# Performance work log

Measured on AMD Instinct MI355X. Metric: run time of the kernel, lower is better.

## Reference

```python
import jax, jax.numpy as jnp
import numpy as np

T, B, IN, OUT = 32, 16, 64, 64
L, W, S = 4096, 64, 3          # mem_length, mem_width, shifting_size
READ_SIZE = W + 3 + S           # k, beta, g, gamma, s
WRITE_SIZE = W + 3 + S + 2 * W  # addressing params + erase + add


def setup_inputs() -> dict:
    key = jax.random.key(0)
    k1, k2 = jax.random.split(key)
    inputs = jax.random.normal(k1, (T, B, IN), dtype=jnp.float32)
    Wc = jax.random.normal(k2, (IN + OUT + W, OUT + READ_SIZE + WRITE_SIZE), dtype=jnp.float32) * 0.05
    bc = jnp.zeros((OUT + READ_SIZE + WRITE_SIZE,), dtype=jnp.float32)
    return {"inputs": inputs, "Wc": Wc, "bc": bc}


def _get_w(params, w_prev, memory):
    # params: [B, W+3+S]; w_prev: [B, L]; memory: [B, L, W]
    k = params[:, :W]
    beta = jax.nn.softplus(params[:, W])[:, None]
    g = jax.nn.sigmoid(params[:, W + 1])[:, None]
    gamma = jax.nn.softplus(params[:, W + 2])[:, None] + 1.0
    s = jax.nn.softmax(params[:, -S:], axis=-1)
    eps = 1e-14
    norm_k = jnp.sqrt(jnp.sum(k * k, axis=-1, keepdims=True) + eps)    # [B,1]
    norm_mem = jnp.sqrt(jnp.sum(memory * memory, axis=-1) + eps)       # [B,L]
    K = jnp.einsum('blw,bw->bl', memory, k) / (norm_mem * norm_k)      # cosine sim
    w_c = jax.nn.softmax(K * beta, axis=-1)
    w_g = w_c * g + (1.0 - g) * w_prev
    # circular shift: w_tilde[i] = sum_j s[j] * w_g[(i + j - left) mod L]
    left = S // 2
    shifted = jnp.stack([jnp.roll(w_g, left - j, axis=1) for j in range(S)], axis=-1)  # [B,L,S]
    w_tilde = jnp.einsum('bls,bs->bl', shifted, s)
    w = jnp.power(w_tilde, gamma)   # sharpen, gamma >= 1
    return w / jnp.sum(w, axis=1, keepdims=True)


def reference(inputs, Wc, bc):
    Bsz = inputs.shape[1]
    r0 = jnp.zeros((Bsz, W), jnp.float32)
    o0 = jnp.zeros((Bsz, OUT), jnp.float32)
    w0 = jnp.zeros((Bsz, L), jnp.float32).at[:, 0].set(1.0)  # one-hot init weights
    m0 = jnp.zeros((Bsz, L, W), jnp.float32)

    def step(carry, x_t):
        r, out, rw, ww, mem = carry
        co = jnp.concatenate([x_t, out, r], axis=1) @ Wc + bc  # linear controller
        out = co[:, :OUT]
        rp = co[:, OUT:OUT + READ_SIZE]
        wp = co[:, -WRITE_SIZE:]
        # read head (uses pre-write memory)
        rw = _get_w(rp, rw, mem)
        r = jnp.einsum('blw,bl->bw', mem, rw)
        # write head: address with same memory, then erase/add
        ww = _get_w(wp[:, :-2 * W], ww, mem)
        e = jax.nn.sigmoid(wp[:, -2 * W:-W])
        a = wp[:, -W:]
        mem = mem * (1.0 - ww[:, :, None] * e[:, None, :]) + ww[:, :, None] * a[:, None, :]
        return (r, out, rw, ww, mem), out

    _, outs = jax.lax.scan(step, (r0, o0, w0, w0, m0), inputs)
    return outs  # [T, B, OUT]
```

## Files before the change

### kernel.cpp

```cpp
#include <hip/hip_runtime.h>

#define T_STEPS 32
#define BATCH   16
#define NBPB    8
#define NBLK    (BATCH * NBPB)
#define NTHR    1024
#define LSL     512
#define MSTR    65
#define NIN     192
#define CO      332

#define OFF_CTR   0
#define OFF_SSUM  512
#define OFF_RSUM  (OFF_SSUM + BATCH * T_STEPS * 4)
#define OFF_HE    (OFF_RSUM + BATCH * T_STEPS * 64)
#define OFF_HP    (OFF_HE + BATCH * T_STEPS * NBPB * 4)
#define COMM_FLOATS (OFF_HP + BATCH * (T_STEPS + 1) * NBPB * 4)

__device__ __forceinline__ float waveSum(float v) {
#pragma unroll
  for (int off = 32; off > 0; off >>= 1) v += __shfl_xor(v, off, 64);
  return v;
}
__device__ __forceinline__ float sigmoidf(float x) { return 1.f / (1.f + __expf(-x)); }
__device__ __forceinline__ float softplusf(float x) { return x > 15.f ? x : log1pf(__expf(x)); }
__device__ __forceinline__ float aload(const float* p) {
  return __hip_atomic_load(p, __ATOMIC_RELAXED, __HIP_MEMORY_SCOPE_AGENT);
}
__device__ __forceinline__ void astore(float* p, float v) {
  __hip_atomic_store(p, v, __ATOMIC_RELAXED, __HIP_MEMORY_SCOPE_AGENT);
}

__device__ __forceinline__ void gbar(unsigned* c, unsigned expected) {
  __syncthreads();
  if (threadIdx.x == 0) {
    atomicAdd(c, 1u);
    while (__hip_atomic_load(c, __ATOMIC_RELAXED, __HIP_MEMORY_SCOPE_AGENT) < expected)
      __builtin_amdgcn_s_sleep(1);
  }
  __syncthreads();
}

__global__ void __launch_bounds__(NTHR, 1) ntm_kernel(
    const float* __restrict__ inp, const float* __restrict__ Wc,
    const float* __restrict__ bcv, float* __restrict__ dout,
    float* __restrict__ comm)
{
  const int b   = blockIdx.x & 15;
  const int g   = blockIdx.x >> 4;
  const int tid = threadIdx.x;
  const int wv  = tid >> 6;
  const int lane = tid & 63;

  __shared__ float mem[LSL * MSTR];
  __shared__ float wpR[LSL], wpW[LSL];
  __shared__ float wbR[LSL], wbW[LSL];
  __shared__ float erR[LSL], erW[LSL];
  __shared__ float xin[NIN], kr[64], kw[64], psc[12], elds[64], alds[64];
  __shared__ float outb[2][64], scrA[16], scrB[16], red[8], rpart[64];
  __shared__ float edge[8], coef[12];

  unsigned* ctr = (unsigned*)comm + b * 32;

  for (int i = tid; i < LSL * MSTR; i += NTHR) mem[i] = 0.f;
  if (tid < LSL) { wpR[tid] = 0.f; wpW[tid] = 0.f; }
  if (g == 0 && tid == 0) { wpR[0] = 1.f; wpW[0] = 1.f; }
  if (tid < 64) { outb[0][tid] = 0.f; outb[1][tid] = 0.f; }
  {
    float* hp0 = comm + OFF_HP + ((size_t)(b * (T_STEPS + 1) + 0) * NBPB + g) * 4;
    if (tid == 0)       { float v = (g == 0) ? 1.f : 0.f; astore(hp0 + 0, v); astore(hp0 + 2, v); }
    if (tid == LSL - 1) { astore(hp0 + 1, 0.f); astore(hp0 + 3, 0.f); }
  }
  unsigned expct = NBPB;
  gbar(ctr, expct);

  for (int t = 0; t < T_STEPS; ++t) {
    float* sS  = comm + OFF_SSUM + (size_t)(b * T_STEPS + t) * 4;
    float* rS  = comm + OFF_RSUM + (size_t)(b * T_STEPS + t) * 64;
    float* hE  = comm + OFF_HE + ((size_t)(b * T_STEPS + t) * NBPB + g) * 4;
    float* hPn = comm + OFF_HP + ((size_t)(b * (T_STEPS + 1) + t + 1) * NBPB + g) * 4;

    if (tid < 64)       xin[tid] = inp[((size_t)t * BATCH + b) * 64 + tid];
    else if (tid < 128) xin[tid] = outb[(t + 1) & 1][tid - 64];
    else if (tid < 192) {
      if (t == 0) xin[tid] = 0.f;
      else {
        const float* sP = comm + OFF_SSUM + (size_t)(b * T_STEPS + t - 1) * 4;
        const float* rP = comm + OFF_RSUM + (size_t)(b * T_STEPS + t - 1) * 64;
        xin[tid] = aload(rP + (tid - 128)) / aload(sP + 2);
      }
    }
    __syncthreads();

    if (tid < 2 * CO) {
      const int col = tid >> 1, h = tid & 1;
      float acc = h ? 0.f : bcv[col];
      const float* wcp = Wc + col + (size_t)(96 * h) * CO;
#pragma unroll 8
      for (int i = 0; i < 96; ++i) acc = fmaf(xin[96 * h + i], wcp[(size_t)i * CO], acc);
      acc += __shfl_xor(acc, 1, 64);
      if (h == 0) {
        if (col < 64) {
          outb[t & 1][col] = acc;
          if (g == 0) dout[((size_t)t * BATCH + b) * 64 + col] = acc;
        }
        else if (col < 128) kr[col - 64] = acc;
        else if (col < 134) psc[col - 128] = acc;
        else if (col < 198) kw[col - 134] = acc;
        else if (col < 204) psc[6 + (col - 198)] = acc;
        else if (col < 268) elds[col - 204] = sigmoidf(acc);
        else                alds[col - 268] = acc;
      }
    }
    __syncthreads();
    if (wv == 0)      { float v = kr[lane]; float s = waveSum(v * v); if (!lane) red[4] = 1.f / sqrtf(s + 1e-14f); }
    else if (wv == 1) { float v = kw[lane]; float s = waveSum(v * v); if (!lane) red[5] = 1.f / sqrtf(s + 1e-14f); }
    else if (wv == 2 && !lane) { red[6] = softplusf(psc[0]); red[7] = softplusf(psc[6]); }
    __syncthreads();

    {
      const float invnkR = red[4], invnkW = red[5];
      const float betaR = red[6], betaW = red[7];
      const int l = tid >> 1, h = tid & 1;
      const int base = l * MSTR + 32 * h;
      const float* krh = kr + 32 * h;
      const float* kwh = kw + 32 * h;
      float ss = 0.f, dr = 0.f, dw = 0.f;
#pragma unroll 8
      for (int i = 0; i < 32; ++i) {
        float v = mem[base + i];
        ss = fmaf(v, v, ss); dr = fmaf(v, krh[i], dr); dw = fmaf(v, kwh[i], dw);
      }
      ss += __shfl_xor(ss, 1, 64);
      dr += __shfl_xor(dr, 1, 64);
      dw += __shfl_xor(dw, 1, 64);
      float rinv = rsqrtf(ss + 1e-14f);
      float eRv = __expf(betaR * (dr * rinv * invnkR - 1.f));
      float eWv = __expf(betaW * (dw * rinv * invnkW - 1.f));
      if (h == 0) {
        erR[l] = eRv; erW[l] = eWv;
        if (l == 0)       { astore(hE + 0, eRv); astore(hE + 2, eWv); }
        if (l == LSL - 1) { astore(hE + 1, eRv); astore(hE + 3, eWv); }
      }
      float sRl = h ? 0.f : eRv, sWl = h ? 0.f : eWv;
      sRl = waveSum(sRl); sWl = waveSum(sWl);
      if (!lane) { scrA[wv] = sRl; scrB[wv] = sWl; }
      __syncthreads();
      if (tid == 0) {
        float a = 0.f, bb = 0.f;
        for (int j = 0; j < 16; ++j) { a += scrA[j]; bb += scrB[j]; }
        atomicAdd(sS + 0, a); atomicAdd(sS + 1, bb);
      }
    }
    expct += NBPB; gbar(ctr, expct);

    {
      const int gm = (g + NBPB - 1) & 7, gp = (g + 1) & 7;
      if (tid == 0) {
        float invSR = 1.f / aload(sS + 0), invSW = 1.f / aload(sS + 1);
        float gR = sigmoidf(psc[1]); coef[0] = gR * invSR; coef[1] = 1.f - gR;
        coef[2] = softplusf(psc[2]) + 1.f;
        float x0 = psc[3], x1 = psc[4], x2 = psc[5];
        float mx = fmaxf(x0, fmaxf(x1, x2));
        float e0 = __expf(x0 - mx), e1 = __expf(x1 - mx), e2 = __expf(x2 - mx);
        float es = 1.f / (e0 + e1 + e2);
        coef[3] = e0 * es; coef[4] = e1 * es; coef[5] = e2 * es;
        float gW = sigmoidf(psc[7]); coef[6] = gW * invSW; coef[7] = 1.f - gW;
        coef[8] = softplusf(psc[8]) + 1.f;
        float y0 = psc[9], y1 = psc[10], y2 = psc[11];
        float my = fmaxf(y0, fmaxf(y1, y2));
        float f0 = __expf(y0 - my), f1 = __expf(y1 - my), f2 = __expf(y2 - my);
        float fs = 1.f / (f0 + f1 + f2);
        coef[9] = f0 * fs; coef[10] = f1 * fs; coef[11] = f2 * fs;
      }
      if (tid == 1) {
        const float* hEm = comm + OFF_HE + ((size_t)(b * T_STEPS + t) * NBPB + gm) * 4;
        const float* hPm = comm + OFF_HP + ((size_t)(b * (T_STEPS + 1) + t) * NBPB + gm) * 4;
        edge[0] = aload(hEm + 1); edge[1] = aload(hEm + 3);
        edge[2] = aload(hPm + 1); edge[3] = aload(hPm + 3);
      }
      if (tid == 2) {
        const float* hEp = comm + OFF_HE + ((size_t)(b * T_STEPS + t) * NBPB + gp) * 4;
        const float* hPp = comm + OFF_HP + ((size_t)(b * (T_STEPS + 1) + t) * NBPB + gp) * 4;
        edge[4] = aload(hEp + 0); edge[5] = aload(hEp + 2);
        edge[6] = aload(hPp + 0); edge[7] = aload(hPp + 2);
      }
      __syncthreads();

      float pRl = 0.f, pWl = 0.f;
      if (tid < LSL) {
        const float aR = coef[0], bR = coef[1], gaR = coef[2];
        const float sr0 = coef[3], sr1 = coef[4], sr2 = coef[5];
        const float aW = coef[6], bW = coef[7], gaW = coef[8];
        const float sw0 = coef[9], sw1 = coef[10], sw2 = coef[11];

        float erm = tid ? erR[tid - 1] : edge[0];
        float ewm = tid ? erW[tid - 1] : edge[1];
        float prm = tid ? wpR[tid - 1] : edge[2];
        float pwm = tid ? wpW[tid - 1] : edge[3];
        float erp = (tid < LSL - 1) ? erR[tid + 1] : edge[4];
        float ewp = (tid < LSL - 1) ? erW[tid + 1] : edge[5];
        float prp = (tid < LSL - 1) ? wpR[tid + 1] : edge[6];
        float pwp = (tid < LSL - 1) ? wpW[tid + 1] : edge[7];

        float wgm = aR * erm + bR * prm;
        float wg0 = aR * erR[tid] + bR * wpR[tid];
        float wgp = aR * erp + bR * prp;
        float wR = __powf(sr0 * wgm + sr1 * wg0 + sr2 * wgp, gaR);
        float vgm = aW * ewm + bW * pwm;
        float vg0 = aW * erW[tid] + bW * wpW[tid];
        float vgp = aW * ewp + bW * pwp;
        float wW = __powf(sw0 * vgm + sw1 * vg0 + sw2 * vgp, gaW);
        wbR[tid] = wR; wbW[tid] = wW;
        pRl = wR; pWl = wW;
      }
      pRl = waveSum(pRl); pWl = waveSum(pWl);
      if (!lane && wv < 8) { scrA[wv] = pRl; scrB[wv] = pWl; }
      __syncthreads();
      if (tid == 0) {
        float a = 0.f, bb = 0.f;
        for (int j = 0; j < 8; ++j) { a += scrA[j]; bb += scrB[j]; }
        atomicAdd(sS + 2, a); atomicAdd(sS + 3, bb);
      }
      float wbv[8];
#pragma unroll
      for (int k = 0; k < 8; ++k) wbv[k] = wbR[lane + 64 * k];
#pragma unroll
      for (int r2 = 0; r2 < 4; ++r2) {
        const int w = wv * 4 + r2;
        float racc = 0.f;
#pragma unroll
        for (int k = 0; k < 8; ++k)
          racc = fmaf(mem[(lane + 64 * k) * MSTR + w], wbv[k], racc);
        racc = waveSum(racc);
        if (!lane) rpart[w] = racc;
      }
      __syncthreads();
      if (tid < 64) atomicAdd(rS + tid, rpart[tid]);
    }
    expct += NBPB; gbar(ctr, expct);

    {
      if (tid == 0) { red[2] = 1.f / aload(sS + 2); red[3] = 1.f / aload(sS + 3); }
      __syncthreads();
      if (tid < LSL) {
        float nR = wbR[tid] * red[2];
        float nW = wbW[tid] * red[3];
        wpR[tid] = nR; wpW[tid] = nW;
        if (tid == 0)       { astore(hPn + 0, nR); astore(hPn + 2, nW); }
        if (tid == LSL - 1) { astore(hPn + 1, nR); astore(hPn + 3, nW); }
      }
      __syncthreads();
      float wwv[8];
#pragma unroll
      for (int k = 0; k < 8; ++k) wwv[k] = wpW[lane + 64 * k];
#pragma unroll
      for (int r2 = 0; r2 < 4; ++r2) {
        const int w = wv * 4 + r2;
        const float e_w = elds[w], a_w = alds[w];
#pragma unroll
        for (int k = 0; k < 8; ++k) {
          const int idx = (lane + 64 * k) * MSTR + w;
          float v = mem[idx];
          float nv = fmaf(v, -(wwv[k] * e_w), v);
          mem[idx] = fmaf(wwv[k], a_w, nv);
        }
      }
    }
  }
}

extern "C" void kernel_launch(void* const* d_in, const int* in_sizes, int n_in,
                              void* d_out, int out_size, void* d_ws, size_t ws_size,
                              hipStream_t stream) {
  const float* inp = (const float*)d_in[0];
  const float* Wc  = (const float*)d_in[1];
  const float* bcv = (const float*)d_in[2];
  float* dout = (float*)d_out;
  float* comm = (float*)d_ws;

  hipMemsetAsync(comm, 0, (size_t)COMM_FLOATS * sizeof(float), stream);

  void* args[] = { (void*)&inp, (void*)&Wc, (void*)&bcv, (void*)&dout, (void*)&comm };
  hipLaunchCooperativeKernel((void*)ntm_kernel, dim3(NBLK), dim3(NTHR),
                             args, 0, stream);
}
```

Measured before the change: 710.8 us.

## Fuse memory write into next step's similarity pass and precompute controller partials

The erase/add memory update is deferred and fused into the next step's row-wise cosine-similarity pass, so memory is read once per step instead of twice. The controller matmul is split: the input and output contributions are precomputed in the previous step's slack, and only the read-vector part runs after the barrier. Keys and erase/add vectors go through a per-block global scratch with double buffering. The read reduction uses a butterfly transpose-reduce with direct atomics instead of a shared-memory staging array. The risks are extra global traffic and correctness subtleties around where the key and erase/add vectors are stored and read.

```diff
diff --git a/kernel.cpp b/kernel.cpp
--- a/kernel.cpp
+++ b/kernel.cpp
@@ -7,15 +7,16 @@
 #define NTHR    1024
 #define LSL     512
 #define MSTR    65
-#define NIN     192
 #define CO      332
 
 #define OFF_CTR   0
 #define OFF_SSUM  512
-#define OFF_RSUM  (OFF_SSUM + BATCH * T_STEPS * 4)
-#define OFF_HE    (OFF_RSUM + BATCH * T_STEPS * 64)
-#define OFF_HP    (OFF_HE + BATCH * T_STEPS * NBPB * 4)
-#define COMM_FLOATS (OFF_HP + BATCH * (T_STEPS + 1) * NBPB * 4)
+#define OFF_RSUM  (OFF_SSUM + BATCH*T_STEPS*4)
+#define OFF_HE    (OFF_RSUM + BATCH*T_STEPS*64)
+#define OFF_HP    (OFF_HE + BATCH*T_STEPS*NBPB*4)
+#define OFF_OUTP  (OFF_HP + BATCH*(T_STEPS+1)*NBPB*4)
+#define OFF_KEA   (OFF_OUTP + NBLK*64)
+#define COMM_FLOATS (OFF_KEA + NBLK*384)
 
 __device__ __forceinline__ float waveSum(float v) {
 #pragma unroll
@@ -46,8 +47,9 @@
     const float* __restrict__ bcv, float* __restrict__ dout,
     float* __restrict__ comm)
 {
-  const int b   = blockIdx.x & 15;
-  const int g   = blockIdx.x >> 4;
+  const int blkid = blockIdx.x;
+  const int b   = blkid & 15;
+  const int g   = blkid >> 4;
   const int tid = threadIdx.x;
   const int wv  = tid >> 6;
   const int lane = tid & 63;
@@ -56,20 +58,28 @@
   __shared__ float wpR[LSL], wpW[LSL];
   __shared__ float wbR[LSL], wbW[LSL];
   __shared__ float erR[LSL], erW[LSL];
-  __shared__ float xin[NIN], kr[64], kw[64], psc[12], elds[64], alds[64];
-  __shared__ float outb[2][64], scrA[16], scrB[16], red[8], rpart[64];
-  __shared__ float edge[8], coef[12];
+  __shared__ float kr[64], kw[64], psc[12], paccT[CO];
+  __shared__ float scrA[16], scrB[16], red[8], coef[12], edge[8];
 
   unsigned* ctr = (unsigned*)comm + b * 32;
+  float* kea = comm + OFF_KEA + blkid * 384;
+  float* outP = comm + OFF_OUTP + blkid * 64;
 
   for (int i = tid; i < LSL * MSTR; i += NTHR) mem[i] = 0.f;
   if (tid < LSL) { wpR[tid] = 0.f; wpW[tid] = 0.f; }
   if (g == 0 && tid == 0) { wpR[0] = 1.f; wpW[0] = 1.f; }
-  if (tid < 64) { outb[0][tid] = 0.f; outb[1][tid] = 0.f; }
+  if (tid < CO) {
+    float acc = bcv[tid];
+    const float* x0 = inp + b * 64;
+    const float* wc = Wc + tid;
+#pragma unroll 8
+    for (int i = 0; i < 64; ++i) acc = fmaf(x0[i], wc[(size_t)i * CO], acc);
+    paccT[tid] = acc;
+  }
   {
-    float* hp0 = comm + OFF_HP + ((size_t)(b * (T_STEPS + 1) + 0) * NBPB + g) * 4;
-    if (tid == 0)       { float v = (g == 0) ? 1.f : 0.f; astore(hp0 + 0, v); astore(hp0 + 2, v); }
-    if (tid == LSL - 1) { astore(hp0 + 1, 0.f); astore(hp0 + 3, 0.f); }
+    float* hp0 = comm + OFF_HP + ((size_t)(b * (T_STEPS + 1)) * NBPB + g) * 4;
+    if (tid == 0) { float v = (g == 0) ? 1.f : 0.f; astore(hp0 + 0, v); astore(hp0 + 2, v); }
+    if (tid == 1) { astore(hp0 + 1, 0.f); astore(hp0 + 3, 0.f); }
   }
   unsigned expct = NBPB;
   gbar(ctr, expct);
@@ -80,36 +90,30 @@
     float* hE  = comm + OFF_HE + ((size_t)(b * T_STEPS + t) * NBPB + g) * 4;
     float* hPn = comm + OFF_HP + ((size_t)(b * (T_STEPS + 1) + t + 1) * NBPB + g) * 4;
 
-    if (tid < 64)       xin[tid] = inp[((size_t)t * BATCH + b) * 64 + tid];
-    else if (tid < 128) xin[tid] = outb[(t + 1) & 1][tid - 64];
-    else if (tid < 192) {
-      if (t == 0) xin[tid] = 0.f;
-      else {
-        const float* sP = comm + OFF_SSUM + (size_t)(b * T_STEPS + t - 1) * 4;
-        const float* rP = comm + OFF_RSUM + (size_t)(b * T_STEPS + t - 1) * 64;
-        xin[tid] = aload(rP + (tid - 128)) / aload(sP + 2);
-      }
-    }
-    __syncthreads();
-
     if (tid < 2 * CO) {
       const int col = tid >> 1, h = tid & 1;
-      float acc = h ? 0.f : bcv[col];
-      const float* wcp = Wc + col + (size_t)(96 * h) * CO;
+      float part = h ? 0.f : paccT[col];
+      if (t > 0) {
+        const float* rSp = comm + OFF_RSUM + (size_t)(b * T_STEPS + t - 1) * 64;
+        const float* sSp = comm + OFF_SSUM + (size_t)(b * T_STEPS + t - 1) * 4;
+        const float invPR = 1.f / aload(sSp + 2);
+        const float* wc = Wc + (size_t)(128 + 32 * h) * CO + col;
+        float racc = 0.f;
 #pragma unroll 8
-      for (int i = 0; i < 96; ++i) acc = fmaf(xin[96 * h + i], wcp[(size_t)i * CO], acc);
-      acc += __shfl_xor(acc, 1, 64);
+        for (int j = 0; j < 32; ++j) racc = fmaf(rSp[32 * h + j], wc[(size_t)j * CO], racc);
+        part = fmaf(racc, invPR, part);
+      }
+      float acc = part + __shfl_xor(part, 1, 64);
       if (h == 0) {
         if (col < 64) {
-          outb[t & 1][col] = acc;
           if (g == 0) dout[((size_t)t * BATCH + b) * 64 + col] = acc;
-        }
-        else if (col < 128) kr[col - 64] = acc;
-        else if (col < 134) psc[col - 128] = acc;
-        else if (col < 198) kw[col - 134] = acc;
-        else if (col < 204) psc[6 + (col - 198)] = acc;
-        else if (col < 268) elds[col - 204] = sigmoidf(acc);
-        else                alds[col - 268] = acc;
+          outP[col] = acc;
+        } else if (col < 128)  { kr[col - 64] = acc;  kea[col - 64] = acc; }
+        else if (col < 134)    psc[col - 128] = acc;
+        else if (col < 198)    { kw[col - 134] = acc; kea[64 + col - 134] = acc; }
+        else if (col < 204)    psc[6 + col - 198] = acc;
+        else if (col < 268)    kea[128 + (t & 1) * 128 + (col - 204)] = sigmoidf(acc);
+        else                   kea[128 + (t & 1) * 128 + 64 + (col - 268)] = acc;
       }
     }
     __syncthreads();
@@ -122,14 +126,29 @@
       const float invnkR = red[4], invnkW = red[5];
       const float betaR = red[6], betaW = red[7];
       const int l = tid >> 1, h = tid & 1;
-      const int base = l * MSTR + 32 * h;
-      const float* krh = kr + 32 * h;
-      const float* kwh = kw + 32 * h;
+      float* mrow = &mem[l * MSTR + 32 * h];
       float ss = 0.f, dr = 0.f, dw = 0.f;
-#pragma unroll 8
-      for (int i = 0; i < 32; ++i) {
-        float v = mem[base + i];
-        ss = fmaf(v, v, ss); dr = fmaf(v, krh[i], dr); dw = fmaf(v, kwh[i], dw);
+      if (t > 0) {
+        const float wWl = wpW[l];
+        const float4* k4p = (const float4*)kea + 8 * h;
+        const float4* w4p = (const float4*)(kea + 64) + 8 * h;
+        const float4* e4p = (const float4*)(kea + 128 + ((t + 1) & 1) * 128) + 8 * h;
+        const float4* a4p = (const float4*)(kea + 128 + ((t + 1) & 1) * 128 + 64) + 8 * h;
+#pragma unroll
+        for (int q = 0; q < 8; ++q) {
+          float4 e4 = e4p[q], a4 = a4p[q], k4 = k4p[q], w4 = w4p[q];
+          float v0 = mrow[4 * q + 0], v1 = mrow[4 * q + 1];
+          float v2 = mrow[4 * q + 2], v3 = mrow[4 * q + 3];
+          v0 = fmaf(wWl, a4.x, fmaf(v0, -(wWl * e4.x), v0));
+          v1 = fmaf(wWl, a4.y, fmaf(v1, -(wWl * e4.y), v1));
+          v2 = fmaf(wWl, a4.z, fmaf(v2, -(wWl * e4.z), v2));
+          v3 = fmaf(wWl, a4.w, fmaf(v3, -(wWl * e4.w), v3));
+          mrow[4 * q + 0] = v0; mrow[4 * q + 1] = v1;
+          mrow[4 * q + 2] = v2; mrow[4 * q + 3] = v3;
+          ss = fmaf(v0, v0, fmaf(v1, v1, fmaf(v2, v2, fmaf(v3, v3, ss))));
+          dr = fmaf(v0, k4.x, fmaf(v1, k4.y, fmaf(v2, k4.z, fmaf(v3, k4.w, dr))));
+          dw = fmaf(v0, w4.x, fmaf(v1, w4.y, fmaf(v2, w4.z, fmaf(v3, w4.w, dw))));
+        }
       }
       ss += __shfl_xor(ss, 1, 64);
       dr += __shfl_xor(dr, 1, 64);
@@ -145,12 +164,12 @@
       float sRl = h ? 0.f : eRv, sWl = h ? 0.f : eWv;
       sRl = waveSum(sRl); sWl = waveSum(sWl);
       if (!lane) { scrA[wv] = sRl; scrB[wv] = sWl; }
-      __syncthreads();
-      if (tid == 0) {
-        float a = 0.f, bb = 0.f;
-        for (int j = 0; j < 16; ++j) { a += scrA[j]; bb += scrB[j]; }
-        atomicAdd(sS + 0, a); atomicAdd(sS + 1, bb);
-      }
+    }
+    __syncthreads();
+    if (tid == 0) {
+      float a = 0.f, bb = 0.f;
+      for (int j = 0; j < 16; ++j) { a += scrA[j]; bb += scrB[j]; }
+      atomicAdd(sS + 0, a); atomicAdd(sS + 1, bb);
     }
     expct += NBPB; gbar(ctr, expct);
 
@@ -193,7 +212,6 @@
         const float sr0 = coef[3], sr1 = coef[4], sr2 = coef[5];
         const float aW = coef[6], bW = coef[7], gaW = coef[8];
         const float sw0 = coef[9], sw1 = coef[10], sw2 = coef[11];
-
         float erm = tid ? erR[tid - 1] : edge[0];
         float ewm = tid ? erW[tid - 1] : edge[1];
         float prm = tid ? wpR[tid - 1] : edge[2];
@@ -202,7 +220,6 @@
         float ewp = (tid < LSL - 1) ? erW[tid + 1] : edge[5];
         float prp = (tid < LSL - 1) ? wpR[tid + 1] : edge[6];
         float pwp = (tid < LSL - 1) ? wpW[tid + 1] : edge[7];
-
         float wgm = aR * erm + bR * prm;
         float wg0 = aR * erR[tid] + bR * wpR[tid];
         float wgp = aR * erp + bR * prp;
@@ -225,48 +242,60 @@
       float wbv[8];
 #pragma unroll
       for (int k = 0; k < 8; ++k) wbv[k] = wbR[lane + 64 * k];
-#pragma unroll
-      for (int r2 = 0; r2 < 4; ++r2) {
-        const int w = wv * 4 + r2;
-        float racc = 0.f;
+      float racc4[4];
+#pragma unroll
+      for (int r = 0; r < 4; ++r) {
+        const int w = 4 * wv + r;
+        float acc = 0.f;
 #pragma unroll
         for (int k = 0; k < 8; ++k)
-          racc = fmaf(mem[(lane + 64 * k) * MSTR + w], wbv[k], racc);
-        racc = waveSum(racc);
-        if (!lane) rpart[w] = racc;
-      }
-      __syncthreads();
-      if (tid < 64) atomicAdd(rS + tid, rpart[tid]);
+          acc = fmaf(mem[(lane + 64 * k) * MSTR + w], wbv[k], acc);
+        racc4[r] = acc;
+      }
+      {
+        const bool u5 = (lane & 32) != 0;
+        float t2[2];
+#pragma unroll
+        for (int j = 0; j < 2; ++j) {
+          float sent = u5 ? racc4[j] : racc4[j + 2];
+          float keep = u5 ? racc4[j + 2] : racc4[j];
+          t2[j] = keep + __shfl_xor(sent, 32, 64);
+        }
+        const bool u4 = (lane & 16) != 0;
+        float sent = u4 ? t2[0] : t2[1];
+        float keep = u4 ? t2[1] : t2[0];
+        float t1 = keep + __shfl_xor(sent, 16, 64);
+        t1 += __shfl_xor(t1, 8, 64);
+        t1 += __shfl_xor(t1, 4, 64);
+        t1 += __shfl_xor(t1, 2, 64);
+        t1 += __shfl_xor(t1, 1, 64);
+        if ((lane & 15) == 0) atomicAdd(rS + 4 * wv + (lane >> 4), t1);
+      }
+      if (tid < CO) {
+        const int tt = (t + 1 < T_STEPS) ? t + 1 : T_STEPS - 1;
+        float acc = bcv[tid];
+        const float* xr = inp + ((size_t)tt * BATCH + b) * 64;
+        const float* wc = Wc + tid;
+#pragma unroll 8
+        for (int i = 0; i < 64; ++i) acc = fmaf(xr[i], wc[(size_t)i * CO], acc);
+        const float* wc2 = Wc + (size_t)64 * CO + tid;
+#pragma unroll 8
+        for (int i = 0; i < 64; ++i) acc = fmaf(outP[i], wc2[(size_t)i * CO], acc);
+        paccT[tid] = acc;
+      }
     }
     expct += NBPB; gbar(ctr, expct);
 
-    {
-      if (tid == 0) { red[2] = 1.f / aload(sS + 2); red[3] = 1.f / aload(sS + 3); }
-      __syncthreads();
-      if (tid < LSL) {
-        float nR = wbR[tid] * red[2];
-        float nW = wbW[tid] * red[3];
-        wpR[tid] = nR; wpW[tid] = nW;
-        if (tid == 0)       { astore(hPn + 0, nR); astore(hPn + 2, nW); }
-        if (tid == LSL - 1) { astore(hPn + 1, nR); astore(hPn + 3, nW); }
-      }
-      __syncthreads();
-      float wwv[8];
-#pragma unroll
-      for (int k = 0; k < 8; ++k) wwv[k] = wpW[lane + 64 * k];
-#pragma unroll
-      for (int r2 = 0; r2 < 4; ++r2) {
-        const int w = wv * 4 + r2;
-        const float e_w = elds[w], a_w = alds[w];
-#pragma unroll
-        for (int k = 0; k < 8; ++k) {
-          const int idx = (lane + 64 * k) * MSTR + w;
-          float v = mem[idx];
-          float nv = fmaf(v, -(wwv[k] * e_w), v);
-          mem[idx] = fmaf(wwv[k], a_w, nv);
-        }
-      }
-    }
+    if (tid == 0) { red[2] = 1.f / aload(sS + 2); red[3] = 1.f / aload(sS + 3); }
+    __syncthreads();
+    if (tid < LSL) {
+      float nR = wbR[tid] * red[2];
+      float nW = wbW[tid] * red[3];
+      wpR[tid] = nR; wpW[tid] = nW;
+      if (tid == 0)       { astore(hPn + 0, nR); astore(hPn + 2, nW); }
+      if (tid == LSL - 1) { astore(hPn + 1, nR); astore(hPn + 3, nW); }
+    }
+    __syncthreads();
   }
 }
 
```

Measured after the change: 1.183 ms. 1.66x slower.
